# Kernel optimization log

Measured on AMD Instinct MI355X. Metric: run time of the kernel, lower is better.

## Reference

```python
import jax, jax.numpy as jnp
from jax import lax
import numpy as np

L2 = 1.0   # regularization_strength for soft_rank
W1 = 1.0   # weight on (1 - spearman)
W2 = 1.0   # weight on BCE-with-logits


def _isotonic_nondecreasing(y):
    """argmin_{v1<=...<=vn} 0.5||v-y||^2 via the min-max (pool means) formula.
    v_i = max_{j<=i} min_{k>=i} mean(y[j..k]). Same solution (and generic
    gradient) as sequential PAV, but fully vectorized / O(n^2)."""
    n = y.shape[0]
    c = jnp.concatenate([jnp.zeros((1,), y.dtype), jnp.cumsum(y)])  # prefix sums
    j = jnp.arange(n)[:, None]
    k = jnp.arange(n)[None, :]
    length = (k - j + 1).astype(y.dtype)
    M = (c[k + 1] - c[j]) / length                    # mean(y[j..k]) for j<=k
    BIG = jnp.asarray(np.finfo(np.float32).max / 4, y.dtype)
    M = jnp.where(j <= k, M, BIG)                     # mask invalid j>k
    S = lax.cummin(M, axis=1, reverse=True)           # S[j,i] = min_{k>=i} M[j,k]
    V = lax.cummax(S, axis=0)                         # V[i,i] = max_{j<=i} S[j,i]
    return jnp.diagonal(V)


def _isotonic_nonincreasing(y):
    # argmin_{v1>=...>=vn} 0.5||v-y||^2  (what fast_soft_sort's isotonic_l2 solves)
    return -_isotonic_nondecreasing(-y)


def _soft_rank_1d(x, reg):
    """fast_soft_sort soft_rank (L2 regularization, ASCENDING) for a 1D vector:
    projection of x/reg onto the permutahedron of w=[n,...,1]."""
    n = x.shape[0]
    theta = x / reg
    w = jnp.arange(n, 0, -1, dtype=x.dtype)           # [n, n-1, ..., 1]
    perm = jnp.argsort(-theta)                        # descending sort
    s = theta[perm]
    dual = _isotonic_nonincreasing(s - w)
    primal = s - dual
    inv = jnp.argsort(perm)
    return primal[inv]


def setup_inputs() -> dict:
    key = jax.random.key(0)
    k1, k2 = jax.random.split(key)
    y_hat = jax.random.normal(k1, (1, 4096), dtype=jnp.float32)   # logits
    y = jax.random.uniform(k2, (1, 4096), dtype=jnp.float32)      # targets in [0,1]
    return {"y_hat": y_hat, "y": y}


def reference(y_hat, y):
    sr = jax.vmap(lambda v: _soft_rank_1d(v, L2))     # rank each row
    p = sr(y_hat)
    t = sr(y)
    p = p - p.mean()
    p = p / jnp.linalg.norm(p)
    t = t - t.mean()
    t = t / jnp.linalg.norm(t)
    spearman = jnp.sum(p * t)
    # BCEWithLogitsLoss (mean reduction): mean(log(1+exp(x)) - x*y), stable form
    bce = jnp.mean(jnp.logaddexp(0.0, y_hat) - y_hat * y)
    return W1 * (1.0 - spearman) + W2 * bce
```

## Files before the change

kernel.cpp:

```cpp
#include <hip/hip_runtime.h>
#include <math.h>

#define N 4096
#define NP1 4097

__global__ __launch_bounds__(256) void rank_kernel(
        const float* __restrict__ yh, const float* __restrict__ yv,
        float* __restrict__ sA, float* __restrict__ sB,
        int* __restrict__ posA, int* __restrict__ posB) {
    int g = blockIdx.x * 256 + threadIdx.x;
    int elem = g >> 3;
    int k = g & 7;
    int row = elem >> 12;
    int i = elem & (N - 1);
    const float* X = row ? yv : yh;
    float x = X[i];
    const float4* X4 = (const float4*)X;
    int cnt = 0;
    int m0 = k * 128;
#pragma unroll 4
    for (int m = m0; m < m0 + 128; ++m) {
        float4 f = X4[m];
        int j = 4 * m;
        cnt += (int)(f.x > x) | ((int)(f.x == x) & (int)((j + 0) < i));
        cnt += (int)(f.y > x) | ((int)(f.y == x) & (int)((j + 1) < i));
        cnt += (int)(f.z > x) | ((int)(f.z == x) & (int)((j + 2) < i));
        cnt += (int)(f.w > x) | ((int)(f.w == x) & (int)((j + 3) < i));
    }
    cnt += __shfl_xor(cnt, 1, 8);
    cnt += __shfl_xor(cnt, 2, 8);
    cnt += __shfl_xor(cnt, 4, 8);
    if (k == 0) {
        if (row) { posB[i] = cnt; sB[cnt] = x; }
        else     { posA[i] = cnt; sA[cnt] = x; }
    }
}

__global__ __launch_bounds__(1024) void finalize_kernel(
        const float* __restrict__ yh, const float* __restrict__ yv,
        const float* __restrict__ sA, const float* __restrict__ sB,
        const int* __restrict__ posA, const int* __restrict__ posB,
        float* __restrict__ out) {
    __shared__ double C[NP1];
    __shared__ float prA[N];
    __shared__ double wtot[16];
    __shared__ unsigned short surv[512];
    __shared__ unsigned short gX[514];
    __shared__ double gY[514];
    __shared__ double wred[16][8];
    __shared__ double CNsh;
    __shared__ int survCnt, Hsh;

    int tid = threadIdx.x;
    int lane = tid & 63;
    int wave = tid >> 6;
    int p0 = tid * 4;

    for (int r = 0; r < 2; ++r) {
        const float* S = r ? sB : sA;
        float* PR = r ? (float*)C : prA;

        float4 s4 = ((const float4*)S)[tid];
        double l0 = (double)s4.x - (double)(N - (p0 + 0));
        double l1 = l0 + ((double)s4.y - (double)(N - (p0 + 1)));
        double l2 = l1 + ((double)s4.z - (double)(N - (p0 + 2)));
        double l3 = l2 + ((double)s4.w - (double)(N - (p0 + 3)));
        double t = l3, incl = l3;
        for (int d = 1; d < 64; d <<= 1) {
            double tmp = __shfl_up(incl, d, 64);
            if (lane >= d) incl += tmp;
        }
        if (lane == 63) wtot[wave] = incl;
        if (tid == 0) survCnt = 0;
        __syncthreads();

        if (wave == 0 && lane < 16) {
            double t2 = wtot[lane], incl2 = t2;
            for (int d = 1; d < 16; d <<= 1) {
                double tmp = __shfl_up(incl2, d, 16);
                if (lane >= d) incl2 += tmp;
            }
            wtot[lane] = incl2 - t2;
        }
        __syncthreads();

        double base = wtot[wave] + (incl - t);
        C[p0 + 1] = base + l0;
        C[p0 + 2] = base + l1;
        C[p0 + 3] = base + l2;
        C[p0 + 4] = base + l3;
        if (tid == 0) C[0] = 0.0;
        if (tid == 1023) CNsh = base + l3;
        __syncthreads();

        {
            double CN = CNsh;
            double eps = 1e-9 * fabs(CN) + 1e-6;
            double lv[4] = {l0, l1, l2, l3};
#pragma unroll
            for (int j = 0; j < 4; ++j) {
                int p = p0 + 1 + j;
                if (p < N) {
                    double chord = CN * ((double)p * (1.0 / (double)N));
                    if (base + lv[j] > chord - eps) {
                        int slot = atomicAdd(&survCnt, 1);
                        if (slot < 512) surv[slot] = (unsigned short)p;
                    }
                }
            }
        }
        __syncthreads();

        if (tid == 0) {
            int k = survCnt; if (k > 512) k = 512;
            for (int a = 1; a < k; ++a) {
                unsigned short v = surv[a]; int b = a - 1;
                while (b >= 0 && surv[b] > v) { surv[b + 1] = surv[b]; --b; }
                surv[b + 1] = v;
            }
            int cnt = 0;
            int xa = 0, xb = 0; double ya = 0.0, yb = 0.0;
            for (int q = 0; q <= k + 1; ++q) {
                int x = (q == 0) ? 0 : (q <= k ? (int)surv[q - 1] : N);
                double cy = (q == 0) ? 0.0 : C[x];
                while (cnt >= 2) {
                    double cr = (double)(xb - xa) * (cy - ya) - (yb - ya) * (double)(x - xa);
                    if (cr >= 0.0) {
                        cnt--;
                        xb = xa; yb = ya;
                        if (cnt >= 2) { xa = gX[cnt - 2]; ya = gY[cnt - 2]; }
                    } else break;
                }
                gX[cnt] = (unsigned short)x; gY[cnt] = cy;
                xa = xb; ya = yb; xb = x; yb = cy;
                cnt++;
            }
            Hsh = cnt;
        }
        __syncthreads();

        {
            int H = Hsh;
            float res[4];
#pragma unroll
            for (int j = 0; j < 4; ++j) {
                int p = p0 + j;
                int a = 0, b = H - 1;
                while (b - a > 1) {
                    int mm = (a + b) >> 1;
                    if ((int)gX[mm] <= p) a = mm; else b = mm;
                }
                double dual = (gY[b] - gY[a]) / (double)((int)gX[b] - (int)gX[a]);
                double sp = (j == 0) ? (double)s4.x : (j == 1) ? (double)s4.y
                           : (j == 2) ? (double)s4.z : (double)s4.w;
                res[j] = (float)(sp - dual + 2048.5);
            }
            ((float4*)PR)[tid] = make_float4(res[0], res[1], res[2], res[3]);
        }
        __syncthreads();
    }

    const float* prB = (const float*)C;
    double Sa = 0, Sb = 0, Saa = 0, Sbb = 0, Sab = 0, Bce = 0;
    {
        int4 pa4 = ((const int4*)posA)[tid];
        int4 pb4 = ((const int4*)posB)[tid];
        float4 xh = ((const float4*)yh)[tid];
        float4 yt = ((const float4*)yv)[tid];
        int pa[4] = {pa4.x, pa4.y, pa4.z, pa4.w};
        int pb[4] = {pb4.x, pb4.y, pb4.z, pb4.w};
        float xx[4] = {xh.x, xh.y, xh.z, xh.w};
        float yy[4] = {yt.x, yt.y, yt.z, yt.w};
#pragma unroll
        for (int j = 0; j < 4; ++j) {
            double a = (double)prA[pa[j]];
            double b = (double)prB[pb[j]];
            Sa += a; Sb += b; Saa += a * a; Sbb += b * b; Sab += a * b;
            float x = xx[j];
            float bt = fmaxf(x, 0.0f) + log1pf(__expf(-fabsf(x))) - x * yy[j];
            Bce += (double)bt;
        }
    }
    for (int d = 32; d; d >>= 1) {
        Sa  += __shfl_xor(Sa, d, 64);  Sb  += __shfl_xor(Sb, d, 64);
        Saa += __shfl_xor(Saa, d, 64); Sbb += __shfl_xor(Sbb, d, 64);
        Sab += __shfl_xor(Sab, d, 64); Bce += __shfl_xor(Bce, d, 64);
    }
    if (lane == 0) {
        wred[wave][0] = Sa;  wred[wave][1] = Sb;  wred[wave][2] = Saa;
        wred[wave][3] = Sbb; wred[wave][4] = Sab; wred[wave][5] = Bce;
    }
    __syncthreads();
    if (tid == 0) {
        double sa = 0, sb = 0, saa = 0, sbb = 0, sab = 0, bce = 0;
        for (int w = 0; w < 16; ++w) {
            sa += wred[w][0]; sb += wred[w][1]; saa += wred[w][2];
            sbb += wred[w][3]; sab += wred[w][4]; bce += wred[w][5];
        }
        double n = (double)N;
        double cov = sab - sa * sb / n;
        double va = saa - sa * sa / n;
        double vb = sbb - sb * sb / n;
        double spearman = cov / sqrt(va * vb);
        out[0] = (float)(1.0 - spearman + bce / n);
    }
}

extern "C" void kernel_launch(void* const* d_in, const int* in_sizes, int n_in,
                              void* d_out, int out_size, void* d_ws, size_t ws_size,
                              hipStream_t stream) {
    const float* yh = (const float*)d_in[0];
    const float* yv = (const float*)d_in[1];
    float* out = (float*)d_out;

    float* sA  = (float*)d_ws;
    float* sB  = sA + N;
    int* posA  = (int*)(sB + N);
    int* posB  = posA + N;

    hipLaunchKernelGGL(rank_kernel, dim3(256), dim3(256), 0, stream,
                       yh, yv, sA, sB, posA, posB);
    hipLaunchKernelGGL(finalize_kernel, dim3(1), dim3(1024), 0, stream,
                       yh, yv, sA, sB, posA, posB, out);
}
```

Measured before the change: 80.95 us.

## Process both rank rows concurrently in finalize kernel with half-block each

```diff
diff --git a/kernel.cpp b/kernel.cpp
--- a/kernel.cpp
+++ b/kernel.cpp
@@ -2,7 +2,6 @@
 #include <math.h>
 
 #define N 4096
-#define NP1 4097
 
 __global__ __launch_bounds__(256) void rank_kernel(
         const float* __restrict__ yh, const float* __restrict__ yv,
@@ -41,126 +40,130 @@
         const float* __restrict__ sA, const float* __restrict__ sB,
         const int* __restrict__ posA, const int* __restrict__ posB,
         float* __restrict__ out) {
-    __shared__ double C[NP1];
-    __shared__ float prA[N];
-    __shared__ double wtot[16];
-    __shared__ unsigned short surv[512];
-    __shared__ unsigned short gX[514];
-    __shared__ double gY[514];
-    __shared__ double wred[16][8];
-    __shared__ double CNsh;
-    __shared__ int survCnt, Hsh;
-
-    int tid = threadIdx.x;
-    int lane = tid & 63;
-    int wave = tid >> 6;
-    int p0 = tid * 4;
-
-    for (int r = 0; r < 2; ++r) {
-        const float* S = r ? sB : sA;
-        float* PR = r ? (float*)C : prA;
-
-        float4 s4 = ((const float4*)S)[tid];
-        double l0 = (double)s4.x - (double)(N - (p0 + 0));
-        double l1 = l0 + ((double)s4.y - (double)(N - (p0 + 1)));
-        double l2 = l1 + ((double)s4.z - (double)(N - (p0 + 2)));
-        double l3 = l2 + ((double)s4.w - (double)(N - (p0 + 3)));
-        double t = l3, incl = l3;
-        for (int d = 1; d < 64; d <<= 1) {
-            double tmp = __shfl_up(incl, d, 64);
-            if (lane >= d) incl += tmp;
-        }
-        if (lane == 63) wtot[wave] = incl;
-        if (tid == 0) survCnt = 0;
-        __syncthreads();
-
-        if (wave == 0 && lane < 16) {
-            double t2 = wtot[lane], incl2 = t2;
-            for (int d = 1; d < 16; d <<= 1) {
-                double tmp = __shfl_up(incl2, d, 16);
-                if (lane >= d) incl2 += tmp;
-            }
-            wtot[lane] = incl2 - t2;
-        }
-        __syncthreads();
-
-        double base = wtot[wave] + (incl - t);
-        C[p0 + 1] = base + l0;
-        C[p0 + 2] = base + l1;
-        C[p0 + 3] = base + l2;
-        C[p0 + 4] = base + l3;
-        if (tid == 0) C[0] = 0.0;
-        if (tid == 1023) CNsh = base + l3;
-        __syncthreads();
-
-        {
-            double CN = CNsh;
-            double eps = 1e-9 * fabs(CN) + 1e-6;
-            double lv[4] = {l0, l1, l2, l3};
-#pragma unroll
-            for (int j = 0; j < 4; ++j) {
-                int p = p0 + 1 + j;
-                if (p < N) {
-                    double chord = CN * ((double)p * (1.0 / (double)N));
-                    if (base + lv[j] > chord - eps) {
-                        int slot = atomicAdd(&survCnt, 1);
-                        if (slot < 512) surv[slot] = (unsigned short)p;
-                    }
-                }
-            }
-        }
-        __syncthreads();
-
-        if (tid == 0) {
-            int k = survCnt; if (k > 512) k = 512;
-            for (int a = 1; a < k; ++a) {
-                unsigned short v = surv[a]; int b = a - 1;
-                while (b >= 0 && surv[b] > v) { surv[b + 1] = surv[b]; --b; }
-                surv[b + 1] = v;
-            }
-            int cnt = 0;
-            int xa = 0, xb = 0; double ya = 0.0, yb = 0.0;
-            for (int q = 0; q <= k + 1; ++q) {
-                int x = (q == 0) ? 0 : (q <= k ? (int)surv[q - 1] : N);
-                double cy = (q == 0) ? 0.0 : C[x];
-                while (cnt >= 2) {
-                    double cr = (double)(xb - xa) * (cy - ya) - (yb - ya) * (double)(x - xa);
-                    if (cr >= 0.0) {
-                        cnt--;
-                        xb = xa; yb = ya;
-                        if (cnt >= 2) { xa = gX[cnt - 2]; ya = gY[cnt - 2]; }
-                    } else break;
-                }
-                gX[cnt] = (unsigned short)x; gY[cnt] = cy;
-                xa = xb; ya = yb; xb = x; yb = cy;
-                cnt++;
-            }
-            Hsh = cnt;
-        }
-        __syncthreads();
-
-        {
-            int H = Hsh;
-            float res[4];
-#pragma unroll
-            for (int j = 0; j < 4; ++j) {
-                int p = p0 + j;
-                int a = 0, b = H - 1;
-                while (b - a > 1) {
-                    int mm = (a + b) >> 1;
-                    if ((int)gX[mm] <= p) a = mm; else b = mm;
-                }
-                double dual = (gY[b] - gY[a]) / (double)((int)gX[b] - (int)gX[a]);
-                double sp = (j == 0) ? (double)s4.x : (j == 1) ? (double)s4.y
-                           : (j == 2) ? (double)s4.z : (double)s4.w;
-                res[j] = (float)(sp - dual + 2048.5);
-            }
-            ((float4*)PR)[tid] = make_float4(res[0], res[1], res[2], res[3]);
-        }
-        __syncthreads();
-    }
-
-    const float* prB = (const float*)C;
+    __shared__ float pr[2][N];
+    __shared__ double wtot[2][8];
+    __shared__ double CNsh[2];
+    __shared__ unsigned short survX[2][512];
+    __shared__ double survY[2][512];
+    __shared__ unsigned short gX[2][516];
+    __shared__ double gY[2][516];
+    __shared__ int survCnt[2];
+    __shared__ int Hsh[2];
+    __shared__ double wred[16][6];
+
+    const int tid  = threadIdx.x;
+    const int lane = tid & 63;
+    const int wave = tid >> 6;
+    const int r    = tid >> 9;
+    const int ht   = tid & 511;
+    const int hw   = wave & 7;
+    const int q0   = ht * 8;
+
+    const float* S = r ? sB : sA;
+    float4 sa4 = ((const float4*)S)[2 * ht];
+    float4 sb4 = ((const float4*)S)[2 * ht + 1];
+    float sv[8] = {sa4.x, sa4.y, sa4.z, sa4.w, sb4.x, sb4.y, sb4.z, sb4.w};
+
+    double m[8];
+    double acc = 0.0;
+#pragma unroll
+    for (int j = 0; j < 8; ++j) {
+        acc += (double)sv[j] - (double)(N - (q0 + j));
+        m[j] = acc;
+    }
+    double tot = m[7], incl = tot;
+#pragma unroll
+    for (int d = 1; d < 64; d <<= 1) {
+        double t = __shfl_up(incl, d, 64);
+        if (lane >= d) incl += t;
+    }
+    if (lane == 63) wtot[r][hw] = incl;
+    if (tid < 2) survCnt[tid] = 0;
+    __syncthreads();
+
+    if (tid < 16) {
+        int rr = tid >> 3, idx = tid & 7;
+        double v = wtot[rr][idx], inc = v;
+#pragma unroll
+        for (int d = 1; d < 8; d <<= 1) {
+            double t = __shfl_up(inc, d, 8);
+            if (idx >= d) inc += t;
+        }
+        wtot[rr][idx] = inc - v;
+        if (idx == 7) CNsh[rr] = inc;
+    }
+    __syncthreads();
+
+    double base = wtot[r][hw] + (incl - tot);
+    double CN = CNsh[r];
+    double eps = 1e-9 * fabs(CN) + 1e-6;
+    const double invN = 1.0 / (double)N;
+
+#pragma unroll
+    for (int j = 0; j < 8; ++j) {
+        int p = q0 + 1 + j;
+        if (p < N) {
+            double cp = base + m[j];
+            if (cp > CN * ((double)p * invN) - eps) {
+                int slot = atomicAdd(&survCnt[r], 1);
+                if (slot < 512) { survX[r][slot] = (unsigned short)p; survY[r][slot] = cp; }
+            }
+        }
+    }
+    __syncthreads();
+
+    if (ht == 0) {
+        int k = survCnt[r]; if (k > 512) k = 512;
+        for (int a = 1; a < k; ++a) {
+            unsigned short vx = survX[r][a]; double vy = survY[r][a];
+            int b = a - 1;
+            while (b >= 0 && survX[r][b] > vx) {
+                survX[r][b + 1] = survX[r][b]; survY[r][b + 1] = survY[r][b]; --b;
+            }
+            survX[r][b + 1] = vx; survY[r][b + 1] = vy;
+        }
+        int cnt = 0;
+        int xa = 0, xb = 0; double ya = 0.0, yb = 0.0;
+        for (int q = 0; q <= k + 1; ++q) {
+            int x; double cy;
+            if (q == 0)      { x = 0; cy = 0.0; }
+            else if (q <= k) { x = (int)survX[r][q - 1]; cy = survY[r][q - 1]; }
+            else             { x = N; cy = CN; }
+            while (cnt >= 2) {
+                double cr = (double)(xb - xa) * (cy - ya) - (yb - ya) * (double)(x - xa);
+                if (cr >= 0.0) {
+                    cnt--; xb = xa; yb = ya;
+                    if (cnt >= 2) { xa = (int)gX[r][cnt - 2]; ya = gY[r][cnt - 2]; }
+                } else break;
+            }
+            gX[r][cnt] = (unsigned short)x; gY[r][cnt] = cy;
+            xa = xb; ya = yb; xb = x; yb = cy;
+            cnt++;
+        }
+        Hsh[r] = cnt;
+    }
+    __syncthreads();
+
+    {
+        int H = Hsh[r];
+        float res[8];
+#pragma unroll
+        for (int j = 0; j < 8; ++j) {
+            int p = q0 + j;
+            int a = 0, b = H - 1;
+            while (b - a > 1) {
+                int mm = (a + b) >> 1;
+                if ((int)gX[r][mm] <= p) a = mm; else b = mm;
+            }
+            double dual = (gY[r][b] - gY[r][a]) / (double)((int)gX[r][b] - (int)gX[r][a]);
+            res[j] = (float)((double)sv[j] - dual - 2048.0);
+        }
+        float4* dst = (float4*)&pr[r][q0];
+        dst[0] = make_float4(res[0], res[1], res[2], res[3]);
+        dst[1] = make_float4(res[4], res[5], res[6], res[7]);
+    }
+    __syncthreads();
+
     double Sa = 0, Sb = 0, Saa = 0, Sbb = 0, Sab = 0, Bce = 0;
     {
         int4 pa4 = ((const int4*)posA)[tid];
@@ -173,14 +176,16 @@
         float yy[4] = {yt.x, yt.y, yt.z, yt.w};
 #pragma unroll
         for (int j = 0; j < 4; ++j) {
-            double a = (double)prA[pa[j]];
-            double b = (double)prB[pb[j]];
+            double a = (double)pr[0][pa[j]];
+            double b = (double)pr[1][pb[j]];
             Sa += a; Sb += b; Saa += a * a; Sbb += b * b; Sab += a * b;
             float x = xx[j];
-            float bt = fmaxf(x, 0.0f) + log1pf(__expf(-fabsf(x))) - x * yy[j];
+            float e = __expf(-fabsf(x));
+            float bt = fmaxf(x, 0.0f) + __logf(1.0f + e) - x * yy[j];
             Bce += (double)bt;
         }
     }
+#pragma unroll
     for (int d = 32; d; d >>= 1) {
         Sa  += __shfl_xor(Sa, d, 64);  Sb  += __shfl_xor(Sb, d, 64);
         Saa += __shfl_xor(Saa, d, 64); Sbb += __shfl_xor(Sbb, d, 64);
```

Measured after the change: 79.03 us. 1.02x faster.
